# Performance work log

Measured on AMD Instinct MI355X. Metric: run time of the kernel, lower is better.

## Reference

```python
import jax, jax.numpy as jnp
import numpy as np

B, S, H = 4, 512, 768
D, M = 24, 96          # hdim_proj_dim, hdim_mlp_hidden
O = 2 * max(128, H // 2)  # val_mlp hidden = 768


def setup_inputs() -> dict:
    key = jax.random.key(0)
    ks = jax.random.split(key, 14)
    u = lambda k, shp, fan_in: jax.random.uniform(k, shp, jnp.float32, -1.0, 1.0) / np.float32(np.sqrt(fan_in))
    return {
        'H_j': jax.random.normal(ks[0], (B, S, H), jnp.float32),
        'H_i': jax.random.normal(ks[1], (B, S, H), jnp.float32),
        'Wpj': u(ks[2], (H, D), H),
        'Wpi': u(ks[3], (H, D), H),
        'Ws1': u(ks[4], (4 * D, M), 4 * D),
        'bs1': u(ks[5], (M,), 4 * D),
        'ws2': u(ks[6], (M,), M),
        'bs2': u(ks[7], (), M),
        'Wv1': u(ks[8], (3 * H, O), 3 * H),
        'bv1': u(ks[9], (O,), 3 * H),
        'Wv2': u(ks[10], (O, H), O),
        'bv2': u(ks[11], (H,), O),
        'alpha': jnp.float32(0.05),
        'attn_mask': jnp.ones((B, S), jnp.int32),
    }


def reference(H_j, H_i, Wpj, Wpi, Ws1, bs1, ws2, bs2, Wv1, bv1, Wv2, bv2, alpha, attn_mask):
    # Projections [B,S,D]
    Zj = H_j @ Wpj
    Zi = H_i @ Wpi
    # 4term score MLP, first layer decomposed over the concat blocks:
    # cat(Zj_p, Zi_p, Zj_p*Zi_p, |Zj_p - Zi_p|) @ Ws1
    W1j, W1i, W1h, W1d = Ws1[:D], Ws1[D:2 * D], Ws1[2 * D:3 * D], Ws1[3 * D:]
    tj = Zj @ W1j                                   # [B,P,M]
    ti = Zi @ W1i                                   # [B,Q,M]
    th = jnp.einsum('bpd,bqd,dm->bpqm', Zj, Zi, W1h)  # hadamard term
    diff = jnp.abs(Zj[:, :, None, :] - Zi[:, None, :, :])  # [B,P,Q,D]
    td = jnp.einsum('bpqd,dm->bpqm', diff, W1d)
    hid = jax.nn.relu(tj[:, :, None, :] + ti[:, None, :, :] + th + td + bs1)  # [B,P,Q,M]
    logits = jnp.einsum('bpqm,m->bpq', hid, ws2) + bs2  # [B,P,Q]
    # mask over source tokens (last dim); token_temp == 1.0 so no division
    mask = attn_mask.astype(logits.dtype)
    logits = logits + (1.0 - mask)[:, None, :] * jnp.finfo(logits.dtype).min
    probs = jax.nn.softmax(logits, axis=-1)
    ctx = jnp.einsum('bpq,bqh->bph', probs, H_i)    # [B,S,H]
    # val_mlp on cat(ctx, H_j, ctx*H_j), first layer decomposed
    Wc, Wj, Wh = Wv1[:H], Wv1[H:2 * H], Wv1[2 * H:]
    mhid = jax.nn.relu(ctx @ Wc + H_j @ Wj + (ctx * H_j) @ Wh + bv1)
    msg = mhid @ Wv2 + bv2
    # dropout is identity in eval mode
    return alpha * msg
```

## Files before the change

### kernel.cpp

```cpp
#include <hip/hip_runtime.h>
#include <hip/hip_bf16.h>

#define Bb 4
#define Ss 512
#define Hh 768
#define Dd 24
#define Mm 96
#define Oo 768

typedef __bf16 bf16x8 __attribute__((ext_vector_type(8)));
typedef __bf16 bf16x4 __attribute__((ext_vector_type(4)));
typedef float f32x4 __attribute__((ext_vector_type(4)));

__device__ __forceinline__ void transpose_tile_v(
    const float* __restrict__ s, __bf16* __restrict__ d,
    int R, int C, int bx, int by, float* smem, int tid)
{
    const int x = tid & 31, y = tid >> 5;
    const int c0 = bx * 32, r0 = by * 32;
    #pragma unroll
    for (int i = 0; i < 4; ++i)
        smem[(y + 8 * i) * 33 + x] = s[(size_t)(r0 + y + 8 * i) * C + c0 + x];
    __syncthreads();
    const int cl = tid >> 3, rg = tid & 7;
    bf16x4 o = { (__bf16)smem[(rg * 4 + 0) * 33 + cl],
                 (__bf16)smem[(rg * 4 + 1) * 33 + cl],
                 (__bf16)smem[(rg * 4 + 2) * 33 + cl],
                 (__bf16)smem[(rg * 4 + 3) * 33 + cl] };
    *(bf16x4*)&d[(size_t)(c0 + cl) * R + r0 + rg * 4] = o;
}

__global__ __launch_bounds__(256) void prep_a(
    const float* __restrict__ Hj, const float* __restrict__ Hi,
    const float* __restrict__ Wpj, const float* __restrict__ Wpi,
    const float* __restrict__ Wv1, const float* __restrict__ Wv2,
    const float* __restrict__ Ws1,
    float* __restrict__ Zj_pad, float* __restrict__ Zi_pad,
    __bf16* __restrict__ Zi_pack, __bf16* __restrict__ B1g,
    __bf16* __restrict__ HiT, __bf16* __restrict__ Wv1T,
    __bf16* __restrict__ Wv2T, __bf16* __restrict__ Acat)
{
    __shared__ float smem[7744];
    const int bid = blockIdx.x;
    const int tid = threadIdx.x;

    if (bid < 512) {
        const int which = bid >> 8;
        const int rowbase = (bid & 255) * 8;
        const float* src = (which ? Hi : Hj) + (size_t)rowbase * Hh;
        const float* W = which ? Wpi : Wpj;
        f32x4* rowbuf4 = (f32x4*)smem;
        float* partial = smem + 6144;

        #pragma unroll
        for (int k2 = 0; k2 < 6; ++k2) {
            const int f = tid + 256 * k2;
            rowbuf4[f] = ((const f32x4*)src)[f];
        }
        __syncthreads();

        if (which == 0) {
            #pragma unroll
            for (int k2 = 0; k2 < 6; ++k2) {
                const int f = tid + 256 * k2;
                const int r = f / 192, kk = f % 192;
                const f32x4 v = rowbuf4[f];
                bf16x4 o = {(__bf16)v[0], (__bf16)v[1], (__bf16)v[2], (__bf16)v[3]};
                *(bf16x4*)&Acat[(size_t)(rowbase + r) * 2304 + Hh + kk * 4] = o;
            }
        } else {
            const int bz = rowbase >> 9, q0 = rowbase & 511;
            __bf16* hb = HiT + (size_t)bz * Hh * Ss + q0;
            #pragma unroll
            for (int k2 = 0; k2 < 3; ++k2) {
                const int h = tid + 256 * k2;
                bf16x8 o;
                #pragma unroll
                for (int r = 0; r < 8; ++r) o[r] = (__bf16)smem[r * Hh + h];
                *(bf16x8*)&hb[(size_t)h * Ss] = o;
            }
        }

        if (tid < 192) {
            const int d = tid % Dd, e = tid / Dd;
            float acc[8];
            #pragma unroll
            for (int r = 0; r < 8; ++r) acc[r] = 0.f;
            const float* Wb = W + (size_t)(e * 96) * Dd + d;
            const f32x4* rb = rowbuf4 + e * 24;
            #pragma unroll 4
            for (int h4 = 0; h4 < 24; ++h4) {
                const float w0 = Wb[(h4 * 4 + 0) * Dd];
                const float w1 = Wb[(h4 * 4 + 1) * Dd];
                const float w2 = Wb[(h4 * 4 + 2) * Dd];
                const float w3 = Wb[(h4 * 4 + 3) * Dd];
                #pragma unroll
                for (int r = 0; r < 8; ++r) {
                    const f32x4 v = rb[r * 192 + h4];
                    acc[r] = fmaf(v[0], w0, acc[r]);
                    acc[r] = fmaf(v[1], w1, acc[r]);
                    acc[r] = fmaf(v[2], w2, acc[r]);
                    acc[r] = fmaf(v[3], w3, acc[r]);
                }
            }
            #pragma unroll
            for (int r = 0; r < 8; ++r) partial[e * 200 + r * 25 + d] = acc[r];
        }
        __syncthreads();
        if (tid < 192) {
            const int r = tid / Dd, d = tid % Dd;
            float z = 0.f;
            #pragma unroll
            for (int e = 0; e < 8; ++e) z += partial[e * 200 + r * 25 + d];
            const int row = rowbase + r;
            (which ? Zi_pad : Zj_pad)[(size_t)row * 32 + d] = z;
            if (which) Zi_pack[(size_t)row * 32 + d] = (__bf16)z;
        } else {
            const int t2 = tid - 192;
            const int r = t2 >> 3, k = 24 + (t2 & 7);
            const int row = rowbase + r;
            (which ? Zi_pad : Zj_pad)[(size_t)row * 32 + k] = 0.f;
            if (which) Zi_pack[(size_t)row * 32 + k] =
                (__bf16)((k == Dd) ? 1.f : 0.f);
        }
    } else if (bid < 2240) {
        const int rem = bid - 512;
        transpose_tile_v(Wv1, Wv1T, 3 * Hh, Oo, rem % 24, rem / 24, smem, tid);
    } else if (bid < 2816) {
        const int rem = bid - 2240;
        transpose_tile_v(Wv2, Wv2T, Oo, Hh, rem % 24, rem / 24, smem, tid);
    } else {
        if (tid < Mm) {
            const int m = tid;
            __bf16 outv[32];
            #pragma unroll
            for (int d = 0; d < Dd; ++d)
                outv[d] = (__bf16)Ws1[(3 * Dd + d) * Mm + m];
            #pragma unroll
            for (int k = Dd; k < 32; ++k) outv[k] = (__bf16)0.f;
            __bf16* dst = B1g + (size_t)m * 32;
            #pragma unroll
            for (int k = 0; k < 4; ++k)
                *(bf16x8*)(dst + k * 8) = *(bf16x8*)&outv[k * 8];
        }
    }
}

__global__ __launch_bounds__(256) void prep_b(
    const float* __restrict__ Zj_pad, const float* __restrict__ Ws1,
    const float* __restrict__ bs1, __bf16* __restrict__ B0all)
{
    const int t = blockIdx.x * 256 + threadIdx.x;
    const int row = t / Mm, m = t % Mm;
    const float* zr = Zj_pad + (size_t)row * 32;
    float zf[Dd];
    #pragma unroll
    for (int k = 0; k < 6; ++k) {
        const f32x4 v = *(const f32x4*)(zr + k * 4);
        zf[k * 4 + 0] = v[0]; zf[k * 4 + 1] = v[1];
        zf[k * 4 + 2] = v[2]; zf[k * 4 + 3] = v[3];
    }
    float ra = bs1[m];
    #pragma unroll
    for (int d = 0; d < Dd; ++d) ra = fmaf(zf[d], Ws1[d * Mm + m], ra);
    __bf16 outv[32];
    #pragma unroll
    for (int d = 0; d < Dd; ++d)
        outv[d] = (__bf16)fmaf(zf[d], Ws1[(2 * Dd + d) * Mm + m],
                               Ws1[(Dd + d) * Mm + m]);
    outv[Dd] = (__bf16)ra;
    #pragma unroll
    for (int k = Dd + 1; k < 32; ++k) outv[k] = (__bf16)0.f;
    __bf16* dst = B0all + ((size_t)row * Mm + m) * 32;
    #pragma unroll
    for (int k = 0; k < 4; ++k)
        *(bf16x8*)(dst + k * 8) = *(bf16x8*)&outv[k * 8];
}

__global__ __launch_bounds__(256, 4) void pair_kernel(
    const float* __restrict__ Zj_pad, const float* __restrict__ Zi_pad,
    const __bf16* __restrict__ Zi_pack, const __bf16* __restrict__ B0all,
    const __bf16* __restrict__ B1g,
    const float* __restrict__ ws2, const float* __restrict__ bs2p,
    const int* __restrict__ mask, __bf16* __restrict__ probs)
{
    const int bp = blockIdx.x;
    const int b  = bp >> 9;
    const int tid  = threadIdx.x;
    const int lane = tid & 63;
    const int wid  = tid >> 6;
    const int col  = lane & 15;
    const int g    = lane >> 4;

    __shared__ float logitsl[Ss];
    __shared__ float red[8];

    float zj8[8];
    {
        const float* zr = Zj_pad + (size_t)bp * 32 + g * 8;
        const float4 u = *(const float4*)zr;
        const float4 v = *(const float4*)(zr + 4);
        zj8[0]=u.x; zj8[1]=u.y; zj8[2]=u.z; zj8[3]=u.w;
        zj8[4]=v.x; zj8[5]=v.y; zj8[6]=v.z; zj8[7]=v.w;
    }

    bf16x8 bw0[6], bw1[6];
    float ws2r[6];
    const __bf16* b0base = B0all + (size_t)bp * Mm * 32;
    #pragma unroll
    for (int n = 0; n < 6; ++n) {
        const int m = n * 16 + col;
        ws2r[n] = ws2[m];
        bw0[n] = *(const bf16x8*)(b0base + (size_t)m * 32 + g * 8);
        bw1[n] = *(const bf16x8*)(B1g + (size_t)m * 32 + g * 8);
    }

    const float*  zipb = Zi_pad  + (size_t)b * Ss * 32;
    const __bf16* zpkb = Zi_pack + (size_t)b * Ss * 32;

    #pragma unroll 2
    for (int t = 0; t < 8; ++t) {
        const int q0 = wid * 128 + t * 16;
        const int q  = q0 + col;
        const bf16x8 a0 = *(const bf16x8*)(zpkb + (size_t)q * 32 + g * 8);
        const float4 u = *(const float4*)(zipb + (size_t)q * 32 + g * 8);
        const float4 v = *(const float4*)(zipb + (size_t)q * 32 + g * 8 + 4);
        bf16x8 a1;
        a1[0]=(__bf16)fabsf(zj8[0]-u.x); a1[1]=(__bf16)fabsf(zj8[1]-u.y);
        a1[2]=(__bf16)fabsf(zj8[2]-u.z); a1[3]=(__bf16)fabsf(zj8[3]-u.w);
        a1[4]=(__bf16)fabsf(zj8[4]-v.x); a1[5]=(__bf16)fabsf(zj8[5]-v.y);
        a1[6]=(__bf16)fabsf(zj8[6]-v.z); a1[7]=(__bf16)fabsf(zj8[7]-v.w);

        f32x4 acc[6];
        #pragma unroll
        for (int n = 0; n < 6; ++n) acc[n] = (f32x4){0.f, 0.f, 0.f, 0.f};
        #pragma unroll
        for (int n = 0; n < 6; ++n) {
            acc[n] = __builtin_amdgcn_mfma_f32_16x16x32_bf16(a0, bw0[n], acc[n], 0, 0, 0);
            acc[n] = __builtin_amdgcn_mfma_f32_16x16x32_bf16(a1, bw1[n], acc[n], 0, 0, 0);
        }

        float lsum[4] = {0.f, 0.f, 0.f, 0.f};
        #pragma unroll
        for (int n = 0; n < 6; ++n)
            #pragma unroll
            for (int r = 0; r < 4; ++r)
                lsum[r] = fmaf(fmaxf(acc[n][r], 0.f), ws2r[n], lsum[r]);
        #pragma unroll
        for (int off = 1; off <= 8; off <<= 1) {
            #pragma unroll
            for (int r = 0; r < 4; ++r) lsum[r] += __shfl_xor(lsum[r], off);
        }
        if (col == 0) {
            float4 o = {lsum[0], lsum[1], lsum[2], lsum[3]};
            *(float4*)&logitsl[q0 + g * 4] = o;
        }
    }
    __syncthreads();

    const float bs2v = bs2p[0];
    const int* mrow = mask + (size_t)b * Ss;
    float l0 = logitsl[tid]       + bs2v + (1.0f - (float)mrow[tid])       * (-3.402823466e+38f);
    float l1 = logitsl[tid + 256] + bs2v + (1.0f - (float)mrow[tid + 256]) * (-3.402823466e+38f);
    float vmax = fmaxf(l0, l1);
    #pragma unroll
    for (int off = 32; off > 0; off >>= 1) vmax = fmaxf(vmax, __shfl_xor(vmax, off));
    if (lane == 0) red[wid] = vmax;
    __syncthreads();
    const float mx = fmaxf(fmaxf(red[0], red[1]), fmaxf(red[2], red[3]));
    const float e0 = __expf(l0 - mx);
    const float e1 = __expf(l1 - mx);
    float vs = e0 + e1;
    #pragma unroll
    for (int off = 32; off > 0; off >>= 1) vs += __shfl_xor(vs, off);
    if (lane == 0) red[4 + wid] = vs;
    __syncthreads();
    const float inv = 1.0f / (red[4] + red[5] + red[6] + red[7]);
    __bf16* prow = probs + (size_t)bp * Ss;
    prow[tid] = (__bf16)(e0 * inv);
    prow[tid + 256] = (__bf16)(e1 * inv);
}

__device__ __forceinline__ void gload16(const __bf16* g, __bf16* l)
{
    __builtin_amdgcn_global_load_lds(
        (const __attribute__((address_space(1))) void*)g,
        (__attribute__((address_space(3))) void*)l, 16, 0, 0);
}

__device__ __forceinline__ int swz(int row, int k)
{
    return row * 64 + (k ^ ((row & 7) << 3));
}

template<int MODE>
__global__ __launch_bounds__(256) void gemm_kernel(
    const __bf16* __restrict__ A, const __bf16* __restrict__ Bt,
    const float* __restrict__ Hjf, const float* __restrict__ bias,
    const float* __restrict__ alphap,
    __bf16* __restrict__ obf, float* __restrict__ of)
{
    constexpr int K = (MODE == 0) ? 512 : (MODE == 1) ? 2304 : 768;
    constexpr int NIT = K / 64;

    __shared__ __align__(16) __bf16 As[3][64 * 64];
    __shared__ __align__(16) __bf16 Bs[3][96 * 64];

    const int tid = threadIdx.x;
    const int lane = tid & 63;
    const int wid = tid >> 6;
    const int col = lane & 15, g = lane >> 4;
    const int wm = wid >> 1, wn = wid & 1;
    const int r0 = blockIdx.x * 64;
    const int n0 = blockIdx.y * 96;
    const __bf16* Btb = (MODE == 0) ? Bt + (size_t)(r0 >> 9) * (Hh * Ss) : Bt;

    const __bf16* asrc[2];
    const __bf16* bsrc[3];
    int aldo[2], bldo[3];
    #pragma unroll
    for (int i = 0; i < 2; ++i) {
        const int c = (wid * 2 + i) * 64 + lane;
        const int row = c >> 3;
        const int k16 = (c & 7) ^ (row & 7);
        asrc[i] = A + (size_t)(r0 + row) * K + k16 * 8;
        aldo[i] = (wid * 2 + i) * 512;
    }
    #pragma unroll
    for (int i = 0; i < 3; ++i) {
        const int c = (wid * 3 + i) * 64 + lane;
        const int row = c >> 3;
        const int k16 = (c & 7) ^ (row & 7);
        bsrc[i] = Btb + (size_t)(n0 + row) * K + k16 * 8;
        bldo[i] = (wid * 3 + i) * 512;
    }

    auto stage = [&](int t, int buf) {
        __bf16* ab = &As[buf][0];
        __bf16* bb = &Bs[buf][0];
        #pragma unroll
        for (int i = 0; i < 2; ++i) gload16(asrc[i] + (size_t)t * 64, ab + aldo[i]);
        #pragma unroll
        for (int i = 0; i < 3; ++i) gload16(bsrc[i] + (size_t)t * 64, bb + bldo[i]);
    };

    f32x4 acc[2][3];
    #pragma unroll
    for (int mi = 0; mi < 2; ++mi)
        #pragma unroll
        for (int ni = 0; ni < 3; ++ni) acc[mi][ni] = (f32x4){0.f, 0.f, 0.f, 0.f};

    stage(0, 0);
    stage(1, 1);

    for (int it = 0; it < NIT; ++it) {
        if (it < NIT - 1) asm volatile("s_waitcnt vmcnt(5)" ::: "memory");
        else              asm volatile("s_waitcnt vmcnt(0)" ::: "memory");
        __builtin_amdgcn_s_barrier();
        __builtin_amdgcn_sched_barrier(0);
        if (it + 2 < NIT) stage(it + 2, (it + 2) % 3);

        const __bf16* Ac = As[it % 3];
        const __bf16* Bc = Bs[it % 3];
        #pragma unroll
        for (int h = 0; h < 2; ++h) {
            const int ka = h * 32 + g * 8;
            const bf16x8 a0 = *(const bf16x8*)&Ac[swz(wm * 32 +      col, ka)];
            const bf16x8 a1 = *(const bf16x8*)&Ac[swz(wm * 32 + 16 + col, ka)];
            const bf16x8 b0 = *(const bf16x8*)&Bc[swz(wn * 48 +      col, ka)];
            const bf16x8 b1 = *(const bf16x8*)&Bc[swz(wn * 48 + 16 + col, ka)];
            const bf16x8 b2 = *(const bf16x8*)&Bc[swz(wn * 48 + 32 + col, ka)];
            acc[0][0] = __builtin_amdgcn_mfma_f32_16x16x32_bf16(a0, b0, acc[0][0], 0, 0, 0);
            acc[0][1] = __builtin_amdgcn_mfma_f32_16x16x32_bf16(a0, b1, acc[0][1], 0, 0, 0);
            acc[0][2] = __builtin_amdgcn_mfma_f32_16x16x32_bf16(a0, b2, acc[0][2], 0, 0, 0);
            acc[1][0] = __builtin_amdgcn_mfma_f32_16x16x32_bf16(a1, b0, acc[1][0], 0, 0, 0);
            acc[1][1] = __builtin_amdgcn_mfma_f32_16x16x32_bf16(a1, b1, acc[1][1], 0, 0, 0);
            acc[1][2] = __builtin_amdgcn_mfma_f32_16x16x32_bf16(a1, b2, acc[1][2], 0, 0, 0);
        }
    }

    const float al = (MODE == 2) ? alphap[0] : 0.f;
    #pragma unroll
    for (int mi = 0; mi < 2; ++mi) {
        #pragma unroll
        for (int r = 0; r < 4; ++r) {
            const int row = r0 + wm * 32 + mi * 16 + g * 4 + r;
            #pragma unroll
            for (int ni = 0; ni < 3; ++ni) {
                const int cn = n0 + wn * 48 + ni * 16 + col;
                const float v = acc[mi][ni][r];
                if (MODE == 0) {
                    const float hjv = Hjf[(size_t)row * Hh + cn];
                    obf[(size_t)row * 2304 + cn] = (__bf16)v;
                    obf[(size_t)row * 2304 + 1536 + cn] = (__bf16)(v * hjv);
                } else if (MODE == 1) {
                    obf[(size_t)row * Oo + cn] = (__bf16)fmaxf(v + bias[cn], 0.f);
                } else {
                    of[(size_t)row * Hh + cn] = al * (v + bias[cn]);
                }
            }
        }
    }
}

extern "C" void kernel_launch(void* const* d_in, const int* in_sizes, int n_in,
                              void* d_out, int out_size, void* d_ws, size_t ws_size,
                              hipStream_t stream)
{
    const float* Hj  = (const float*)d_in[0];
    const float* Hi  = (const float*)d_in[1];
    const float* Wpj = (const float*)d_in[2];
    const float* Wpi = (const float*)d_in[3];
    const float* Ws1 = (const float*)d_in[4];
    const float* bs1 = (const float*)d_in[5];
    const float* ws2 = (const float*)d_in[6];
    const float* bs2 = (const float*)d_in[7];
    const float* Wv1 = (const float*)d_in[8];
    const float* bv1 = (const float*)d_in[9];
    const float* Wv2 = (const float*)d_in[10];
    const float* bv2 = (const float*)d_in[11];
    const float* alpha = (const float*)d_in[12];
    const int* mask  = (const int*)d_in[13];

    float* ws = (float*)d_ws;
    float* Zj_pad  = ws;
    float* Zi_pad  = Zj_pad + 65536;
    float* Zpack_f = Zi_pad + 65536;
    float* B1_f    = Zpack_f + 32768;
    float* B0_f    = B1_f + 1536;
    float* probs_f = B0_f + 3145728;
    float* HiT_f   = probs_f + 524288;
    float* Wv2T_f  = HiT_f + 786432;
    float* mhid_f  = Wv2T_f + 294912;
    float* Acat_f  = mhid_f + 786432;
    float* Wv1T_f  = Acat_f + 2359296;

    __bf16* Zi_pack  = (__bf16*)Zpack_f;
    __bf16* B1g      = (__bf16*)B1_f;
    __bf16* B0all    = (__bf16*)B0_f;
    __bf16* probs_bf = (__bf16*)probs_f;
    __bf16* HiT      = (__bf16*)HiT_f;
    __bf16* Wv2T     = (__bf16*)Wv2T_f;
    __bf16* mhid_bf  = (__bf16*)mhid_f;
    __bf16* Acat     = (__bf16*)Acat_f;
    __bf16* Wv1T     = (__bf16*)Wv1T_f;

    prep_a<<<dim3(2817), 256, 0, stream>>>(
        Hj, Hi, Wpj, Wpi, Wv1, Wv2, Ws1,
        Zj_pad, Zi_pad, Zi_pack, B1g, HiT, Wv1T, Wv2T, Acat);
    prep_b<<<dim3(768), 256, 0, stream>>>(Zj_pad, Ws1, bs1, B0all);
    pair_kernel<<<dim3(Bb * Ss), 256, 0, stream>>>(
        Zj_pad, Zi_pad, Zi_pack, B0all, B1g, ws2, bs2, mask, probs_bf);
    gemm_kernel<0><<<dim3(2048 / 64, Hh / 96), 256, 0, stream>>>(
        probs_bf, HiT, Hj, nullptr, nullptr, Acat, nullptr);
    gemm_kernel<1><<<dim3(2048 / 64, Oo / 96), 256, 0, stream>>>(
        Acat, Wv1T, nullptr, bv1, nullptr, mhid_bf, nullptr);
    gemm_kernel<2><<<dim3(2048 / 64, Hh / 96), 256, 0, stream>>>(
        mhid_bf, Wv2T, nullptr, bv2, alpha, nullptr, (float*)d_out);
}
```

Before: 190.3 us.

## Fuse per-row score MLP weight construction into pair kernel, drop prep_b

Removes the prep_b kernel and the B1g construction in prep_a. Each pair_kernel block now builds its own bf16 B operands directly from Ws1, bs1 and Zj. Lane group 3 computes the linear-term bias row, and the other groups compute the hadamard+Zi and |diff| weight fragments. This avoids writing and re-reading a large B0all buffer (about 12MB) and saves one kernel launch, at the cost of redundant Ws1 gathers and FMAs in every pair block. The shuffle reduction width is also narrowed to 16.

```diff
diff --git a/kernel.cpp b/kernel.cpp
--- a/kernel.cpp
+++ b/kernel.cpp
@@ -34,9 +34,8 @@
     const float* __restrict__ Hj, const float* __restrict__ Hi,
     const float* __restrict__ Wpj, const float* __restrict__ Wpi,
     const float* __restrict__ Wv1, const float* __restrict__ Wv2,
-    const float* __restrict__ Ws1,
     float* __restrict__ Zj_pad, float* __restrict__ Zi_pad,
-    __bf16* __restrict__ Zi_pack, __bf16* __restrict__ B1g,
+    __bf16* __restrict__ Zi_pack,
     __bf16* __restrict__ HiT, __bf16* __restrict__ Wv1T,
     __bf16* __restrict__ Wv2T, __bf16* __restrict__ Acat)
 {
@@ -126,61 +125,16 @@
     } else if (bid < 2240) {
         const int rem = bid - 512;
         transpose_tile_v(Wv1, Wv1T, 3 * Hh, Oo, rem % 24, rem / 24, smem, tid);
-    } else if (bid < 2816) {
+    } else {
         const int rem = bid - 2240;
         transpose_tile_v(Wv2, Wv2T, Oo, Hh, rem % 24, rem / 24, smem, tid);
-    } else {
-        if (tid < Mm) {
-            const int m = tid;
-            __bf16 outv[32];
-            #pragma unroll
-            for (int d = 0; d < Dd; ++d)
-                outv[d] = (__bf16)Ws1[(3 * Dd + d) * Mm + m];
-            #pragma unroll
-            for (int k = Dd; k < 32; ++k) outv[k] = (__bf16)0.f;
-            __bf16* dst = B1g + (size_t)m * 32;
-            #pragma unroll
-            for (int k = 0; k < 4; ++k)
-                *(bf16x8*)(dst + k * 8) = *(bf16x8*)&outv[k * 8];
-        }
-    }
-}
-
-__global__ __launch_bounds__(256) void prep_b(
-    const float* __restrict__ Zj_pad, const float* __restrict__ Ws1,
-    const float* __restrict__ bs1, __bf16* __restrict__ B0all)
-{
-    const int t = blockIdx.x * 256 + threadIdx.x;
-    const int row = t / Mm, m = t % Mm;
-    const float* zr = Zj_pad + (size_t)row * 32;
-    float zf[Dd];
-    #pragma unroll
-    for (int k = 0; k < 6; ++k) {
-        const f32x4 v = *(const f32x4*)(zr + k * 4);
-        zf[k * 4 + 0] = v[0]; zf[k * 4 + 1] = v[1];
-        zf[k * 4 + 2] = v[2]; zf[k * 4 + 3] = v[3];
-    }
-    float ra = bs1[m];
-    #pragma unroll
-    for (int d = 0; d < Dd; ++d) ra = fmaf(zf[d], Ws1[d * Mm + m], ra);
-    __bf16 outv[32];
-    #pragma unroll
-    for (int d = 0; d < Dd; ++d)
-        outv[d] = (__bf16)fmaf(zf[d], Ws1[(2 * Dd + d) * Mm + m],
-                               Ws1[(Dd + d) * Mm + m]);
-    outv[Dd] = (__bf16)ra;
-    #pragma unroll
-    for (int k = Dd + 1; k < 32; ++k) outv[k] = (__bf16)0.f;
-    __bf16* dst = B0all + ((size_t)row * Mm + m) * 32;
-    #pragma unroll
-    for (int k = 0; k < 4; ++k)
-        *(bf16x8*)(dst + k * 8) = *(bf16x8*)&outv[k * 8];
+    }
 }
 
 __global__ __launch_bounds__(256, 4) void pair_kernel(
     const float* __restrict__ Zj_pad, const float* __restrict__ Zi_pad,
-    const __bf16* __restrict__ Zi_pack, const __bf16* __restrict__ B0all,
-    const __bf16* __restrict__ B1g,
+    const __bf16* __restrict__ Zi_pack,
+    const float* __restrict__ Ws1, const float* __restrict__ bs1,
     const float* __restrict__ ws2, const float* __restrict__ bs2p,
     const int* __restrict__ mask, __bf16* __restrict__ probs)
 {
@@ -206,13 +160,43 @@
 
     bf16x8 bw0[6], bw1[6];
     float ws2r[6];
-    const __bf16* b0base = B0all + (size_t)bp * Mm * 32;
-    #pragma unroll
-    for (int n = 0; n < 6; ++n) {
-        const int m = n * 16 + col;
-        ws2r[n] = ws2[m];
-        bw0[n] = *(const bf16x8*)(b0base + (size_t)m * 32 + g * 8);
-        bw1[n] = *(const bf16x8*)(B1g + (size_t)m * 32 + g * 8);
+    if (g < 3) {
+        #pragma unroll
+        for (int n = 0; n < 6; ++n) {
+            const int m = n * 16 + col;
+            ws2r[n] = ws2[m];
+            bf16x8 b0, b1;
+            #pragma unroll
+            for (int j = 0; j < 8; ++j) {
+                const int d = g * 8 + j;
+                b0[j] = (__bf16)fmaf(zj8[j], Ws1[(2 * Dd + d) * Mm + m],
+                                     Ws1[(Dd + d) * Mm + m]);
+                b1[j] = (__bf16)Ws1[(3 * Dd + d) * Mm + m];
+            }
+            bw0[n] = b0; bw1[n] = b1;
+        }
+    } else {
+        float zf[Dd];
+        const float* zr = Zj_pad + (size_t)bp * 32;
+        #pragma unroll
+        for (int k = 0; k < 6; ++k) {
+            const f32x4 v = *(const f32x4*)(zr + k * 4);
+            zf[k * 4 + 0] = v[0]; zf[k * 4 + 1] = v[1];
+            zf[k * 4 + 2] = v[2]; zf[k * 4 + 3] = v[3];
+        }
+        #pragma unroll
+        for (int n = 0; n < 6; ++n) {
+            const int m = n * 16 + col;
+            ws2r[n] = ws2[m];
+            float ra = bs1[m];
+            #pragma unroll
+            for (int d = 0; d < Dd; ++d) ra = fmaf(zf[d], Ws1[d * Mm + m], ra);
+            bf16x8 b0, b1;
+            #pragma unroll
+            for (int j = 0; j < 8; ++j) { b0[j] = (__bf16)0.f; b1[j] = (__bf16)0.f; }
+            b0[0] = (__bf16)ra;
+            bw0[n] = b0; bw1[n] = b1;
+        }
     }
 
     const float*  zipb = Zi_pad  + (size_t)b * Ss * 32;
@@ -249,7 +233,7 @@
         #pragma unroll
         for (int off = 1; off <= 8; off <<= 1) {
             #pragma unroll
-            for (int r = 0; r < 4; ++r) lsum[r] += __shfl_xor(lsum[r], off);
+            for (int r = 0; r < 4; ++r) lsum[r] += __shfl_xor(lsum[r], off, 16);
         }
         if (col == 0) {
             float4 o = {lsum[0], lsum[1], lsum[2], lsum[3]};
@@ -426,9 +410,7 @@
     float* Zj_pad  = ws;
     float* Zi_pad  = Zj_pad + 65536;
     float* Zpack_f = Zi_pad + 65536;
-    float* B1_f    = Zpack_f + 32768;
-    float* B0_f    = B1_f + 1536;
-    float* probs_f = B0_f + 3145728;
+    float* probs_f = Zpack_f + 32768;
     float* HiT_f   = probs_f + 524288;
     float* Wv2T_f  = HiT_f + 786432;
     float* mhid_f  = Wv2T_f + 294912;
@@ -436,8 +418,6 @@
     float* Wv1T_f  = Acat_f + 2359296;
 
     __bf16* Zi_pack  = (__bf16*)Zpack_f;
-    __bf16* B1g      = (__bf16*)B1_f;
-    __bf16* B0all    = (__bf16*)B0_f;
     __bf16* probs_bf = (__bf16*)probs_f;
     __bf16* HiT      = (__bf16*)HiT_f;
     __bf16* Wv2T     = (__bf16*)Wv2T_f;
@@ -445,12 +425,11 @@
     __bf16* Acat     = (__bf16*)Acat_f;
     __bf16* Wv1T     = (__bf16*)Wv1T_f;
 
-    prep_a<<<dim3(2817), 256, 0, stream>>>(
-        Hj, Hi, Wpj, Wpi, Wv1, Wv2, Ws1,
-        Zj_pad, Zi_pad, Zi_pack, B1g, HiT, Wv1T, Wv2T, Acat);
-    prep_b<<<dim3(768), 256, 0, stream>>>(Zj_pad, Ws1, bs1, B0all);
+    prep_a<<<dim3(2816), 256, 0, stream>>>(
+        Hj, Hi, Wpj, Wpi, Wv1, Wv2,
+        Zj_pad, Zi_pad, Zi_pack, HiT, Wv1T, Wv2T, Acat);
     pair_kernel<<<dim3(Bb * Ss), 256, 0, stream>>>(
-        Zj_pad, Zi_pad, Zi_pack, B0all, B1g, ws2, bs2, mask, probs_bf);
+        Zj_pad, Zi_pad, Zi_pack, Ws1, bs1, ws2, bs2, mask, probs_bf);
     gemm_kernel<0><<<dim3(2048 / 64, Hh / 96), 256, 0, stream>>>(
         probs_bf, HiT, Hj, nullptr, nullptr, Acat, nullptr);
     gemm_kernel<1><<<dim3(2048 / 64, Oo / 96), 256, 0, stream>>>(
```

Result: no change. 193.9 us (+1.9%).
